# Kernel optimization log

Hardware: AMD Instinct MI355X
Metric: run time of the kernel (lower is better)

Reference implementation:

```python
import jax, jax.numpy as jnp
import numpy as np

SPARSITY = 0.01  # sparsity_threshold (softshrink lambda)


def _cas(n):
    # Hartley cas kernel: cos + sin
    t = jnp.arange(n, dtype=jnp.float32)
    a = 2.0 * jnp.pi * jnp.outer(t, t) / n
    return jnp.cos(a) + jnp.sin(a)


def _dht2d(x):
    # Faithful to source 4-D branch: transforms the LAST TWO axes (W and C)
    B, H, W, C = x.shape
    y = jnp.einsum('bhwc,cd->bhwd', x, _cas(C))          # contract channel axis
    return jnp.einsum('vw,bhwd->bhvd', _cas(W), y)       # contract width axis


def setup_inputs() -> dict:
    key = jax.random.key(0)
    k0, k1, k2, k3, k4 = jax.random.split(key, 5)
    B, H, W, C = 1, 180, 360, 512
    nb, bs, f = 8, 64, 1  # num_blocks, block_size, hidden_size_factor
    scale = 0.02
    x = jax.random.normal(k0, (B, H, W, C), jnp.float32)
    w1 = scale * jax.random.normal(k1, (2, nb, bs, bs * f), jnp.float32)
    b1 = scale * jax.random.normal(k2, (2, nb, bs * f), jnp.float32)
    w2 = scale * jax.random.normal(k3, (2, nb, bs * f, bs), jnp.float32)
    b2 = scale * jax.random.normal(k4, (2, nb, bs), jnp.float32)
    return {"x": x, "w1": w1, "b1": b1, "w2": w2, "b2": b2}


def reference(x, w1, b1, w2, b2):
    bias = x
    B, H, W, C = x.shape
    nb, bs = w1.shape[1], w1.shape[2]

    xh = _dht2d(x).reshape(B, H, W, nb, bs)                       # X_H_k
    xn = jnp.roll(jnp.flip(xh, axis=(1, 2)), shift=(1, 1), axis=(1, 2))  # X_H_{-k}

    # layer 1: 0.5*(Xk(w0+w1) + Xn(w0-w1)) + b  (algebraic regroup of the 4 einsums)
    w1a, w1b = w1[0] + w1[1], w1[0] - w1[1]
    o1k = jax.nn.relu(0.5 * (jnp.einsum('bhwki,kio->bhwko', xh, w1a)
                             + jnp.einsum('bhwki,kio->bhwko', xn, w1b)) + b1[0])
    o1n = jax.nn.relu(0.5 * (jnp.einsum('bhwki,kio->bhwko', xn, w1a)
                             + jnp.einsum('bhwki,kio->bhwko', xh, w1b)) + b1[1])

    # layer 2 (faithfully reproduces source bug: o2n consumes o2k, bias included)
    w2a, w2b = w2[0] + w2[1], w2[0] - w2[1]
    o2k = 0.5 * (jnp.einsum('bhwki,kio->bhwko', o1k, w2a)
                 + jnp.einsum('bhwki,kio->bhwko', o1n, w2b)) + b2[0]
    o2n = 0.5 * (jnp.einsum('bhwki,kio->bhwko', o1n, w2a)
                 + jnp.einsum('bhwki,kio->bhwko', o2k, w2b)) + b2[1]

    y = (o2k + o2n).reshape(B, H, W, C)
    y = jnp.sign(y) * jax.nn.relu(jnp.abs(y) - SPARSITY)          # softshrink
    y = _dht2d(y) / (W * C)                                       # idht2d normalization
    return y + bias
```

## Files before the change

kernel.cpp:

```cpp
#include <hip/hip_runtime.h>
#include <math.h>

#define HH 180
#define WDIM 360
#define CDIM 512
#define NP 64800
#define PL 184320

typedef unsigned short u16;
typedef __attribute__((ext_vector_type(8))) short short8;
typedef __attribute__((ext_vector_type(4))) float f4;

__device__ __forceinline__ u16 f2bf(float f){
    unsigned u = __float_as_uint(f);
    return (u16)((u + 0x7fffu + ((u >> 16) & 1u)) >> 16);
}
__device__ __forceinline__ void gl_lds16(const void* g, void* l){
    __builtin_amdgcn_global_load_lds((const __attribute__((address_space(1))) void*)g,
                                     (__attribute__((address_space(3))) void*)l, 16, 0, 0);
}

__global__ void prep(const float* __restrict__ w1, const float* __restrict__ w2,
                     u16* __restrict__ casC, u16* __restrict__ casW, u16* __restrict__ wts)
{
    int idx = blockIdx.x * 256 + threadIdx.x;
    if (idx < 512*512){
        int i = idx >> 9, j = idx & 511;
        int m = (i * j) & 511;
        float a = (float)m * (6.283185307179586f / 512.0f);
        float s, c; __sincosf(a, &s, &c);
        casC[idx] = f2bf(c + s);
    }
    if (idx < 360*384){
        int i = idx / 384, j = idx - (idx / 384) * 384;
        u16 v = 0;
        if (j < 360){
            int m = (i * j) % 360;
            float a = (float)m * (6.283185307179586f / 360.0f);
            float s, c; __sincosf(a, &s, &c);
            v = f2bf(c + s);
        }
        casW[idx] = v;
    }
    if (idx < 131072){
        int s = idx >> 15, r = idx & 32767;
        int kb = r >> 12, o = (r >> 6) & 63, ii = r & 63;
        const float* w = (s < 2) ? w1 : w2;
        float v0 = w[kb*4096 + ii*64 + o];
        float v1 = w[32768 + kb*4096 + ii*64 + o];
        float v = 0.5f * ((s & 1) ? (v0 - v1) : (v0 + v1));
        wts[idx] = f2bf(v);
    }
}

__global__ __launch_bounds__(256)
void cvt_k(const float* __restrict__ x, u16* __restrict__ xb)
{
    long long i = ((long long)blockIdx.x * 256 + threadIdx.x) * 8;
    float4 a = *(const float4*)(x + i);
    float4 b = *(const float4*)(x + i + 4);
    uint4 w;
    w.x = (unsigned)f2bf(a.x) | ((unsigned)f2bf(a.y) << 16);
    w.y = (unsigned)f2bf(a.z) | ((unsigned)f2bf(a.w) << 16);
    w.z = (unsigned)f2bf(b.x) | ((unsigned)f2bf(b.y) << 16);
    w.w = (unsigned)f2bf(b.z) | ((unsigned)f2bf(b.w) << 16);
    *(uint4*)(xb + i) = w;
}

template<int STORE, int SWAP>
__global__ __launch_bounds__(256)
void gemm_k(const u16* __restrict__ A, int ldA, long long sA, int clampA,
            const u16* __restrict__ B, int ldB, long long sB,
            void* __restrict__ C, long long sC, int Mreal,
            const float* __restrict__ X, float scale, int nK, int nbx)
{
    __shared__ u16 As[3][4096];
    __shared__ u16 Bs[3][4096];

    const int tid = threadIdx.x, wv = tid >> 6, l = tid & 63;
    const int l16 = l & 15, quad = l >> 4;
    const int z = blockIdx.z;

    int bx, by;
    if constexpr (SWAP){
        int n = gridDim.x;
        int q = n >> 3, r = n & 7;
        int xcd = blockIdx.x & 7, idx = blockIdx.x >> 3;
        int swz = (xcd < r ? xcd*(q+1) : r*(q+1) + (xcd-r)*q) + idx;
        bx = swz / nbx;
        by = swz - bx * nbx;
    } else {
        bx = blockIdx.x;
        by = blockIdx.y;
    }
    const int row0 = bx * 128, col0 = by * 128;

    const int rh = wv & 1, c0 = wv >> 1;

    const u16* gB = B + sB * z + (long long)(col0 + rh*64 + l) * ldB;
    int ar = row0 + rh*64 + l; ar = ar <= clampA ? ar : clampA;
    const u16* gA = A + sA * z + (long long)ar * ldA;

    f4 acc[4][4];
    #pragma unroll
    for (int mt = 0; mt < 4; ++mt)
        #pragma unroll
        for (int nt = 0; nt < 4; ++nt)
            acc[mt][nt] = (f4)0.0f;

    const int mrow = (wv >> 1) * 64, ncol = (wv & 1) * 64;

    #define STAGE(buf, kt) do{ const int k0_ = (kt)*32;                          \
        gl_lds16(gB + k0_ + c0*8,     &Bs[buf][c0*1024     + rh*512]);           \
        gl_lds16(gB + k0_ + (c0+2)*8, &Bs[buf][(c0+2)*1024 + rh*512]);           \
        gl_lds16(gA + k0_ + c0*8,     &As[buf][c0*1024     + rh*512]);           \
        gl_lds16(gA + k0_ + (c0+2)*8, &As[buf][(c0+2)*1024 + rh*512]); }while(0)

    STAGE(0, 0);
    STAGE(1, 1);
    STAGE(2, 2);

    int cur = 0;
    for (int kt = 0; kt < nK; ++kt){
        asm volatile("s_waitcnt vmcnt(8)" ::: "memory");
        __builtin_amdgcn_s_barrier();
        __builtin_amdgcn_sched_barrier(0);

        short8 af[4];
        #pragma unroll
        for (int mt = 0; mt < 4; ++mt)
            af[mt] = *(const short8*)&As[cur][quad*1024 + (mrow + mt*16 + l16)*8];
        #pragma unroll
        for (int nt = 0; nt < 4; ++nt){
            short8 bfv = *(const short8*)&Bs[cur][quad*1024 + (ncol + nt*16 + l16)*8];
            #pragma unroll
            for (int mt = 0; mt < 4; ++mt)
                acc[mt][nt] = __builtin_amdgcn_mfma_f32_16x16x32_bf16(af[mt], bfv, acc[mt][nt], 0, 0, 0);
        }

        __builtin_amdgcn_sched_barrier(0);
        __builtin_amdgcn_s_barrier();
        __builtin_amdgcn_sched_barrier(0);

        int nxt = kt + 3; if (nxt > nK - 1) nxt = nK - 1;
        STAGE(cur, nxt);
        cur = (cur == 2) ? 0 : cur + 1;
    }
    #undef STAGE

    #pragma unroll
    for (int mt = 0; mt < 4; ++mt){
        #pragma unroll
        for (int i = 0; i < 4; ++i){
            int gr = row0 + mrow + mt*16 + quad*4 + i;
            if (gr >= Mreal) continue;
            int th = 0, tw = 0;
            if constexpr (STORE == 1){ th = gr / 360; tw = gr - th * 360; }
            #pragma unroll
            for (int nt = 0; nt < 4; ++nt){
                int gc = col0 + ncol + nt*16 + l16;
                if constexpr (STORE == 0){
                    ((u16*)C)[sC*z + (long long)gr*512 + gc] = f2bf(acc[mt][nt][i]);
                } else if constexpr (STORE == 1){
                    ((u16*)C)[((long long)th*512 + gc)*360 + tw] = f2bf(acc[mt][nt][i]);
                } else {
                    long long off = sC*z + (long long)gr*512 + gc;
                    ((float*)C)[off] = fmaf(acc[mt][nt][i], scale, X[off]);
                }
            }
        }
    }
}

__global__ __launch_bounds__(256)
void mlp_k(const u16* __restrict__ xh, const u16* __restrict__ wts,
           const float* __restrict__ b1, const float* __restrict__ b2,
           u16* __restrict__ yout)
{
    __shared__ u16 sW0[64*72], sW1[64*72];
    __shared__ u16 sXh[64*72], sXn[64*72], s1k[64*72], s1n[64*72];
    __shared__ float sb[256];

    const int tid = threadIdx.x;
    const int wv = tid >> 6, l = tid & 63, lane16 = l & 15, quad = l >> 4;
    const int kb = blockIdx.y;
    const int p0 = blockIdx.x * 64;
    const int w16 = wv * 16;

    if (tid < 64){
        sb[tid]       = b1[kb*64 + tid];
        sb[64 + tid]  = b1[512 + kb*64 + tid];
        sb[128 + tid] = b2[kb*64 + tid];
        sb[192 + tid] = b2[512 + kb*64 + tid];
    }
    {
        const int r = tid >> 2, sg = (tid & 3) * 16;
        const u16* s0 = wts + kb*4096 + r*64 + sg;
        const u16* s1 = wts + 32768 + kb*4096 + r*64 + sg;
        *(uint4*)&sW0[r*72 + sg]     = *(const uint4*)s0;
        *(uint4*)&sW0[r*72 + sg + 8] = *(const uint4*)(s0 + 8);
        *(uint4*)&sW1[r*72 + sg]     = *(const uint4*)s1;
        *(uint4*)&sW1[r*72 + sg + 8] = *(const uint4*)(s1 + 8);

        int p = p0 + r; int pc = p <= 64799 ? p : 64799;
        int h = pc / 360; int v = pc - h * 360;
        int hn = (h == 0) ? 0 : (180 - h);
        int vn = (v == 0) ? 0 : (360 - v);
        long long bh = (long long)pc * 512 + kb*64 + sg;
        long long bn = (long long)(hn*360 + vn) * 512 + kb*64 + sg;
        *(uint4*)&sXh[r*72 + sg]     = *(const uint4*)&xh[bh];
        *(uint4*)&sXh[r*72 + sg + 8] = *(const uint4*)&xh[bh + 8];
        *(uint4*)&sXn[r*72 + sg]     = *(const uint4*)&xh[bn];
        *(uint4*)&sXn[r*72 + sg + 8] = *(const uint4*)&xh[bn + 8];
    }
    __syncthreads();

    f4 aK[4], aN[4];
    #pragma unroll
    for (int nt = 0; nt < 4; ++nt){ aK[nt] = (f4)0.0f; aN[nt] = (f4)0.0f; }
    #pragma unroll
    for (int kq = 0; kq < 2; ++kq){
        short8 fxh = *(const short8*)&sXh[(w16 + lane16)*72 + kq*32 + quad*8];
        short8 fxn = *(const short8*)&sXn[(w16 + lane16)*72 + kq*32 + quad*8];
        #pragma unroll
        for (int nt = 0; nt < 4; ++nt){
            short8 wa = *(const short8*)&sW0[(nt*16 + lane16)*72 + kq*32 + quad*8];
            short8 wb = *(const short8*)&sW1[(nt*16 + lane16)*72 + kq*32 + quad*8];
            aK[nt] = __builtin_amdgcn_mfma_f32_16x16x32_bf16(fxh, wa, aK[nt], 0,0,0);
            aK[nt] = __builtin_amdgcn_mfma_f32_16x16x32_bf16(fxn, wb, aK[nt], 0,0,0);
            aN[nt] = __builtin_amdgcn_mfma_f32_16x16x32_bf16(fxn, wa, aN[nt], 0,0,0);
            aN[nt] = __builtin_amdgcn_mfma_f32_16x16x32_bf16(fxh, wb, aN[nt], 0,0,0);
        }
    }
    #pragma unroll
    for (int nt = 0; nt < 4; ++nt){
        int cc = nt*16 + lane16;
        #pragma unroll
        for (int i = 0; i < 4; ++i){
            int rr = w16 + quad*4 + i;
            float vk = fmaxf(aK[nt][i] + sb[cc], 0.f);
            float vn = fmaxf(aN[nt][i] + sb[64 + cc], 0.f);
            s1k[rr*72 + cc] = f2bf(vk);
            s1n[rr*72 + cc] = f2bf(vn);
        }
    }
    __syncthreads();

    {
        const int r = tid >> 2, sg = (tid & 3) * 16;
        const u16* s0 = wts + 65536 + kb*4096 + r*64 + sg;
        const u16* s1 = wts + 98304 + kb*4096 + r*64 + sg;
        *(uint4*)&sW0[r*72 + sg]     = *(const uint4*)s0;
        *(uint4*)&sW0[r*72 + sg + 8] = *(const uint4*)(s0 + 8);
        *(uint4*)&sW1[r*72 + sg]     = *(const uint4*)s1;
        *(uint4*)&sW1[r*72 + sg + 8] = *(const uint4*)(s1 + 8);
    }
    __syncthreads();

    f4 k2[4];
    #pragma unroll
    for (int nt = 0; nt < 4; ++nt) k2[nt] = (f4)0.0f;
    #pragma unroll
    for (int kq = 0; kq < 2; ++kq){
        short8 a1k = *(const short8*)&s1k[(w16 + lane16)*72 + kq*32 + quad*8];
        short8 a1n = *(const short8*)&s1n[(w16 + lane16)*72 + kq*32 + quad*8];
        #pragma unroll
        for (int nt = 0; nt < 4; ++nt){
            short8 wa = *(const short8*)&sW0[(nt*16 + lane16)*72 + kq*32 + quad*8];
            short8 wb = *(const short8*)&sW1[(nt*16 + lane16)*72 + kq*32 + quad*8];
            k2[nt] = __builtin_amdgcn_mfma_f32_16x16x32_bf16(a1k, wa, k2[nt], 0,0,0);
            k2[nt] = __builtin_amdgcn_mfma_f32_16x16x32_bf16(a1n, wb, k2[nt], 0,0,0);
        }
    }
    #pragma unroll
    for (int nt = 0; nt < 4; ++nt){
        int cc = nt*16 + lane16;
        #pragma unroll
        for (int i = 0; i < 4; ++i){
            int rr = w16 + quad*4 + i;
            float v2 = k2[nt][i] + sb[128 + cc];
            k2[nt][i] = v2;
            sXh[rr*72 + cc] = f2bf(v2);
        }
    }
    __syncthreads();

    f4 n2[4];
    #pragma unroll
    for (int nt = 0; nt < 4; ++nt) n2[nt] = (f4)0.0f;
    #pragma unroll
    for (int kq = 0; kq < 2; ++kq){
        short8 a1n = *(const short8*)&s1n[(w16 + lane16)*72 + kq*32 + quad*8];
        short8 a2k = *(const short8*)&sXh[(w16 + lane16)*72 + kq*32 + quad*8];
        #pragma unroll
        for (int nt = 0; nt < 4; ++nt){
            short8 wa = *(const short8*)&sW0[(nt*16 + lane16)*72 + kq*32 + quad*8];
            short8 wb = *(const short8*)&sW1[(nt*16 + lane16)*72 + kq*32 + quad*8];
            n2[nt] = __builtin_amdgcn_mfma_f32_16x16x32_bf16(a1n, wa, n2[nt], 0,0,0);
            n2[nt] = __builtin_amdgcn_mfma_f32_16x16x32_bf16(a2k, wb, n2[nt], 0,0,0);
        }
    }
    #pragma unroll
    for (int nt = 0; nt < 4; ++nt){
        int cc = nt*16 + lane16;
        #pragma unroll
        for (int i = 0; i < 4; ++i){
            int rr = w16 + quad*4 + i;
            int p = p0 + rr;
            float y = k2[nt][i] + n2[nt][i] + sb[192 + cc];
            float ay = fabsf(y) - 0.01f;
            float r0 = ay > 0.f ? (y > 0.f ? ay : -ay) : 0.f;
            if (p < 64800) yout[(long long)p * 512 + kb*64 + cc] = f2bf(r0);
        }
    }
}

extern "C" void kernel_launch(void* const* d_in, const int* in_sizes, int n_in,
                              void* d_out, int out_size, void* d_ws, size_t ws_size,
                              hipStream_t stream) {
    const float* x  = (const float*)d_in[0];
    const float* w1 = (const float*)d_in[1];
    const float* b1 = (const float*)d_in[2];
    const float* w2 = (const float*)d_in[3];
    const float* b2 = (const float*)d_in[4];
    float* out = (float*)d_out;

    u16* ws   = (u16*)d_ws;
    u16* casC = ws;
    u16* casW = casC + 262144;
    u16* wts  = casW + 138240;
    u16* bufT = wts  + 131072;
    u16* bufP = bufT + 33177664;

    prep<<<1024, 256, 0, stream>>>(w1, w2, casC, casW, wts);
    cvt_k<<<16200, 256, 0, stream>>>(x, bufP);

    dim3 gBig(2028, 1, 1);
    dim3 gW(3, 4, 180);
    dim3 gM(1013, 8, 1);

    gemm_k<1,1><<<gBig, 256, 0, stream>>>(bufP, 512, 0, 64799,
                                          casC, 512, 0,
                                          bufT, 0, 64800, nullptr, 0.f, 16, 4);
    gemm_k<0,0><<<gW, 256, 0, stream>>>(casW, 384, 0, 359,
                                        bufT, 360, (long long)PL,
                                        bufP, (long long)PL, 360, nullptr, 0.f, 12, 1);
    mlp_k<<<gM, 256, 0, stream>>>(bufP, wts, b1, b2, bufT);
    gemm_k<1,1><<<gBig, 256, 0, stream>>>(bufT, 512, 0, 64799,
                                          casC, 512, 0,
                                          bufP, 0, 64800, nullptr, 0.f, 16, 4);
    gemm_k<2,0><<<gW, 256, 0, stream>>>(casW, 384, 0, 359,
                                        bufP, 360, (long long)PL,
                                        out, (long long)PL, 360,
                                        x, 1.0f/184320.0f, 12, 1);
}
```

Measured before the change: 772.2 us.

## Add dedicated W-axis Hartley GEMM keeping cas matrix resident in LDS

Replaces the generic gemm_k used for the width-axis transform with a specialized wgemm_k. Each 512-thread block loads its full 128x384 slice of the casW matrix into LDS once, then processes 5 consecutive H-slices. It streams the transposed activation tiles through a double buffer with direct global-to-LDS loads and a block-index swizzle. This is meant to remove repeated A-tile loads and improve MFMA utilisation for the two W-axis GEMMs. It also zero-fills padding past the buffers, because B loads may read beyond the last slice; the cost is heavy LDS use (about 128KB per block), which limits occupancy.

```diff
diff --git a/kernel.cpp b/kernel.cpp
--- a/kernel.cpp
+++ b/kernel.cpp
@@ -21,9 +21,11 @@
 }
 
 __global__ void prep(const float* __restrict__ w1, const float* __restrict__ w2,
-                     u16* __restrict__ casC, u16* __restrict__ casW, u16* __restrict__ wts)
+                     u16* __restrict__ casC, u16* __restrict__ casW, u16* __restrict__ wts,
+                     u16* __restrict__ padT, u16* __restrict__ padP)
 {
     int idx = blockIdx.x * 256 + threadIdx.x;
+    if (idx < 64){ padT[idx] = 0; padP[idx] = 0; }
     if (idx < 512*512){
         int i = idx >> 9, j = idx & 511;
         int m = (i * j) & 511;
@@ -172,6 +174,118 @@
     }
 }
 
+template<int STORE>
+__global__ __launch_bounds__(512)
+void wgemm_k(const u16* __restrict__ A, const u16* __restrict__ Bsrc,
+             void* __restrict__ C, const float* __restrict__ X, float scale)
+{
+    __shared__ u16 As[49152];
+    __shared__ u16 Bs[2][8192];
+
+    const int tid = threadIdx.x, wv = tid >> 6, l = tid & 63;
+    const int l16 = l & 15, quad = l >> 4;
+
+    const int q = gridDim.x >> 3;
+    const int swz = (blockIdx.x & 7) * q + (blockIdx.x >> 3);
+    const int bx = swz % 3;
+    const int g  = swz / 3;
+    const int zs = g % 36, by = g / 36;
+    const int row0 = bx * 128, col0 = by * 256, z0 = zs * 5;
+
+    const int wm = wv >> 2, wn = wv & 3;
+    const int mrow = wm * 64, ncol = wn * 64;
+
+    #pragma unroll
+    for (int j = 0; j < 12; ++j){
+        int s = wv + 8*j;
+        int kt = s >> 3, c = (s >> 1) & 3, half = s & 1;
+        int gr = row0 + half*64 + l; gr = gr <= 359 ? gr : 359;
+        gl_lds16(A + (long long)gr*384 + kt*32 + c*8,
+                 &As[kt*4096 + c*1024 + half*512]);
+    }
+
+    #define WSTAGE(buf, t) do{                                                     \
+        int z_ = z0 + (t)/12, kt_ = (t) - ((t)/12)*12;                             \
+        const u16* zb_ = Bsrc + (long long)z_ * PL + kt_*32;                       \
+        int s0_ = wv*2,   c0_ = s0_ >> 2, q0_ = s0_ & 3;                           \
+        gl_lds16(zb_ + (long long)(col0 + q0_*64 + l)*360 + c0_*8,                 \
+                 &Bs[buf][c0_*2048 + q0_*512]);                                    \
+        int s1_ = wv*2+1, c1_ = s1_ >> 2, q1_ = s1_ & 3;                           \
+        gl_lds16(zb_ + (long long)(col0 + q1_*64 + l)*360 + c1_*8,                 \
+                 &Bs[buf][c1_*2048 + q1_*512]); }while(0)
+
+    WSTAGE(0, 0);
+    WSTAGE(1, 1);
+
+    f4 acc[4][4];
+    #pragma unroll
+    for (int mt = 0; mt < 4; ++mt)
+        #pragma unroll
+        for (int nt = 0; nt < 4; ++nt)
+            acc[mt][nt] = (f4)0.0f;
+
+    const int T = 60;
+    int kt = 0, buf = 0, zi = 0;
+    for (int t = 0; t < T; ++t){
+        asm volatile("s_waitcnt vmcnt(2)" ::: "memory");
+        __builtin_amdgcn_s_barrier();
+        __builtin_amdgcn_sched_barrier(0);
+
+        short8 af[4];
+        #pragma unroll
+        for (int mt = 0; mt < 4; ++mt)
+            af[mt] = *(const short8*)&As[kt*4096 + quad*1024 + (mrow + mt*16 + l16)*8];
+        #pragma unroll
+        for (int nt = 0; nt < 4; ++nt){
+            short8 bfv = *(const short8*)&Bs[buf][quad*2048 + (ncol + nt*16 + l16)*8];
+            #pragma unroll
+            for (int mt = 0; mt < 4; ++mt)
+                acc[mt][nt] = __builtin_amdgcn_mfma_f32_16x16x32_bf16(af[mt], bfv, acc[mt][nt], 0, 0, 0);
+        }
+
+        __builtin_amdgcn_sched_barrier(0);
+        __builtin_amdgcn_s_barrier();
+        __builtin_amdgcn_sched_barrier(0);
+
+        int nxt = t + 2; if (nxt > T - 1) nxt = T - 1;
+        WSTAGE(buf, nxt);
+
+        if (kt == 11){
+            const int z = z0 + zi;
+            #pragma unroll
+            for (int mt = 0; mt < 4; ++mt){
+                #pragma unroll
+                for (int i = 0; i < 4; ++i){
+                    int gr = row0 + mrow + mt*16 + quad*4 + i;
+                    if (gr < 360){
+                        long long base = ((long long)z*360 + gr)*512;
+                        #pragma unroll
+                        for (int nt = 0; nt < 4; ++nt){
+                            int gc = col0 + ncol + nt*16 + l16;
+                            if constexpr (STORE == 0){
+                                ((u16*)C)[base + gc] = f2bf(acc[mt][nt][i]);
+                            } else {
+                                ((float*)C)[base + gc] = fmaf(acc[mt][nt][i], scale, X[base + gc]);
+                            }
+                        }
+                    }
+                }
+            }
+            #pragma unroll
+            for (int mt = 0; mt < 4; ++mt)
+                #pragma unroll
+                for (int nt = 0; nt < 4; ++nt)
+                    acc[mt][nt] = (f4)0.0f;
+            ++zi;
+            kt = 0;
+        } else {
+            ++kt;
+        }
+        buf ^= 1;
+    }
+    #undef WSTAGE
+}
+
 __global__ __launch_bounds__(256)
 void mlp_k(const u16* __restrict__ xh, const u16* __restrict__ wts,
            const float* __restrict__ b1, const float* __restrict__ b2,
@@ -332,25 +446,21 @@
     u16* bufT = wts  + 131072;
     u16* bufP = bufT + 33177664;
 
-    prep<<<1024, 256, 0, stream>>>(w1, w2, casC, casW, wts);
+    prep<<<1024, 256, 0, stream>>>(w1, w2, casC, casW, wts,
+                                   bufT + 33177600, bufP + 33177600);
     cvt_k<<<16200, 256, 0, stream>>>(x, bufP);
 
     dim3 gBig(2028, 1, 1);
-    dim3 gW(3, 4, 180);
+    dim3 gWg(216, 1, 1);
     dim3 gM(1013, 8, 1);
 
     gemm_k<1,1><<<gBig, 256, 0, stream>>>(bufP, 512, 0, 64799,
                                           casC, 512, 0,
                                           bufT, 0, 64800, nullptr, 0.f, 16, 4);
-    gemm_k<0,0><<<gW, 256, 0, stream>>>(casW, 384, 0, 359,
-                                        bufT, 360, (long long)PL,
-                                        bufP, (long long)PL, 360, nullptr, 0.f, 12, 1);
+    wgemm_k<0><<<gWg, 512, 0, stream>>>(casW, bufT, bufP, nullptr, 0.f);
     mlp_k<<<gM, 256, 0, stream>>>(bufP, wts, b1, b2, bufT);
     gemm_k<1,1><<<gBig, 256, 0, stream>>>(bufT, 512, 0, 64799,
                                           casC, 512, 0,
                                           bufP, 0, 64800, nullptr, 0.f, 16, 4);
-    gemm_k<2,0><<<gW, 256, 0, stream>>>(casW, 384, 0, 359,
-                                        bufP, 360, (long long)PL,
-                                        out, (long long)PL, 360,
-                                        x, 1.0f/184320.0f, 12, 1);
-}
+    wgemm_k<2><<<gWg, 512, 0, stream>>>(casW, bufP, out, x, 1.0f/184320.0f);
+}
```

Result: no change. 759.6 us (-1.6%).
